# Optimization experiments

Measured on AMD Instinct MI355X. Metric: run time of the kernel, lower is better.

The kernel has to match this reference:

```python
import jax, jax.numpy as jnp
import numpy as np

EPS = 1e-08
N_HEADS = 8
WORD = 128
N_CELLS = 16384
BATCH = 16


def setup_inputs() -> dict:
    key = jax.random.key(0)
    k1, k2 = jax.random.split(key)
    memory = jax.random.normal(k1, (BATCH, N_CELLS, WORD), dtype=jnp.float32)
    controls = jax.random.normal(k2, (BATCH, N_HEADS * (WORD + 6)), dtype=jnp.float32)
    read_dist_bias = jnp.zeros((1, N_HEADS, N_CELLS), dtype=jnp.float32)
    return {"memory": memory, "controls": controls, "read_dist_bias": read_dist_bias}


def _split_controls(controls):
    # order: keys [B,H,W], betas [B,H,1], gates [B,H,1], shifts [B,H,3], gammas [B,H,1]
    B = controls.shape[0]
    pos = 0
    parts = []
    for size in (WORD, 1, 1, 3, 1):
        n = N_HEADS * size
        parts.append(controls[:, pos:pos + n].reshape(B, N_HEADS, size))
        pos += n
    return parts


def _circular_convolution(weights, shifts):
    # out[i] = w[(i-1)%C]*s0 + w[i]*s1 + w[(i+1)%C]*s2  (torch conv2d = cross-correlation)
    return (shifts[..., 0:1] * jnp.roll(weights, 1, axis=-1)
            + shifts[..., 1:2] * weights
            + shifts[..., 2:3] * jnp.roll(weights, -1, axis=-1))


def reference(memory, controls, read_dist_bias):
    keys, betas, gates, shifts, gammas = _split_controls(controls)
    keys = jnp.tanh(keys)                      # [B,H,W]
    betas = jax.nn.softplus(betas)             # [B,H,1]
    gates = jax.nn.sigmoid(gates)              # [B,H,1]
    shifts = jax.nn.softmax(shifts, axis=-1)   # [B,H,3]
    gammas = 1.0 + jax.nn.softplus(gammas)     # [B,H,1]

    # prev weights on a fresh sequence: softmax of the learned bias
    prev_weights = jax.nn.softmax(
        jnp.broadcast_to(read_dist_bias, (memory.shape[0], N_HEADS, N_CELLS)), axis=-1)

    # cosine similarity, [B,H,C]
    dots = jnp.einsum('bcw,bhw->bhc', memory, keys)
    norm = jnp.linalg.norm(keys, axis=-1)[..., None] * jnp.linalg.norm(memory, axis=-1)[:, None, :]
    scores = dots / (norm + EPS)

    w_content = jax.nn.softmax(scores * betas, axis=-1)
    w_interp = gates * w_content + (1.0 - gates) * prev_weights
    w_shift = _circular_convolution(w_interp, shifts)
    w_sharp = w_shift ** gammas
    read_dist = w_sharp / (jnp.sum(w_sharp, axis=-1, keepdims=True) + EPS)

    # read: [B,H,W]
    read_data = jnp.einsum('bhc,bcw->bhw', read_dist, memory)
    return read_data
```

## Files before the change

### kernel.cpp

```cpp
#include <hip/hip_runtime.h>

#define BATCH 16
#define HEADS 8
#define WORD  128
#define CELLS 16384
#define CTRL  1072
#define CB    256

__device__ __forceinline__ float softplusf(float x) {
  return (x > 20.f) ? x : log1pf(expf(x));
}

template<int OP>
__device__ __forceinline__ float block_reduce(float v, float* scratch) {
  #pragma unroll
  for (int o = 32; o > 0; o >>= 1) {
    float u = __shfl_xor(v, o, 64);
    v = OP ? fmaxf(v, u) : (v + u);
  }
  const int t = threadIdx.x;
  __syncthreads();
  if ((t & 63) == 0) scratch[t >> 6] = v;
  __syncthreads();
  if (t < 64) {
    v = (t < 16) ? scratch[t] : (OP ? -3.4e38f : 0.f);
    #pragma unroll
    for (int o = 8; o > 0; o >>= 1) {
      float u = __shfl_xor(v, o, 64);
      v = OP ? fmaxf(v, u) : (v + u);
    }
    if (t == 0) scratch[0] = v;
  }
  __syncthreads();
  v = scratch[0];
  __syncthreads();
  return v;
}

__global__ __launch_bounds__(256)
void scores_kernel(const float* __restrict__ mem,
                   const float* __restrict__ ctrl,
                   float* __restrict__ scores) {
  const int b = blockIdx.y;
  const int c = blockIdx.x * 256 + threadIdx.x;
  const int t = threadIdx.x;

  __shared__ float kk[HEADS * WORD];
  __shared__ float kn[HEADS];

  for (int i = t; i < HEADS * WORD; i += 256)
    kk[i] = tanhf(ctrl[b * CTRL + i]);
  __syncthreads();
  if (t < HEADS) {
    float s = 0.f;
    for (int w = 0; w < WORD; ++w) { float v = kk[t * WORD + w]; s += v * v; }
    kn[t] = sqrtf(s);
  }
  __syncthreads();

  float dot[HEADS];
  #pragma unroll
  for (int h = 0; h < HEADS; ++h) dot[h] = 0.f;
  float nm = 0.f;

  const float4* mrow = (const float4*)&mem[((size_t)b * CELLS + c) * WORD];
  const float4* k4   = (const float4*)kk;
  for (int w4 = 0; w4 < WORD / 4; ++w4) {
    float4 m = mrow[w4];
    nm = fmaf(m.x, m.x, fmaf(m.y, m.y, fmaf(m.z, m.z, fmaf(m.w, m.w, nm))));
    #pragma unroll
    for (int h = 0; h < HEADS; ++h) {
      float4 k = k4[h * (WORD / 4) + w4];
      dot[h] = fmaf(m.x, k.x, fmaf(m.y, k.y, fmaf(m.z, k.z, fmaf(m.w, k.w, dot[h]))));
    }
  }
  nm = sqrtf(nm);
  #pragma unroll
  for (int h = 0; h < HEADS; ++h)
    scores[((size_t)(b * HEADS + h)) * CELLS + c] = dot[h] / (kn[h] * nm + 1e-8f);
}

__global__ __launch_bounds__(1024)
void weights_kernel(const float* __restrict__ scores,
                    const float* __restrict__ ctrl,
                    const float* __restrict__ bias,
                    float* __restrict__ rd) {
  const int bh = blockIdx.x;
  const int b = bh >> 3, h = bh & 7;
  const int t = threadIdx.x;

  __shared__ float buf[CELLS];

  const float* cb = ctrl + b * CTRL;
  const float beta  = softplusf(cb[1024 + h]);
  const float gate  = 1.f / (1.f + expf(-cb[1032 + h]));
  float s0 = cb[1040 + h * 3 + 0];
  float s1 = cb[1040 + h * 3 + 1];
  float s2 = cb[1040 + h * 3 + 2];
  {
    float sm = fmaxf(s0, fmaxf(s1, s2));
    float e0 = expf(s0 - sm), e1 = expf(s1 - sm), e2 = expf(s2 - sm);
    float inv = 1.f / (e0 + e1 + e2);
    s0 = e0 * inv; s1 = e1 * inv; s2 = e2 * inv;
  }
  const float gamma = 1.f + softplusf(cb[1064 + h]);

  float x[16];
  const float* srow = scores + (size_t)bh * CELLS;
  #pragma unroll
  for (int i = 0; i < 16; ++i) x[i] = srow[t + i * 1024] * beta;
  float mx = x[0];
  #pragma unroll
  for (int i = 1; i < 16; ++i) mx = fmaxf(mx, x[i]);
  mx = block_reduce<1>(mx, buf);
  float se = 0.f;
  #pragma unroll
  for (int i = 0; i < 16; ++i) { x[i] = expf(x[i] - mx); se += x[i]; }
  se = block_reduce<0>(se, buf);

  float y[16];
  const float* brow = bias + (size_t)h * CELLS;
  #pragma unroll
  for (int i = 0; i < 16; ++i) y[i] = brow[t + i * 1024];
  float mb = y[0];
  #pragma unroll
  for (int i = 1; i < 16; ++i) mb = fmaxf(mb, y[i]);
  mb = block_reduce<1>(mb, buf);
  float sb = 0.f;
  #pragma unroll
  for (int i = 0; i < 16; ++i) { y[i] = expf(y[i] - mb); sb += y[i]; }
  sb = block_reduce<0>(sb, buf);

  const float a1 = gate / se;
  const float a2 = (1.f - gate) / sb;
  #pragma unroll
  for (int i = 0; i < 16; ++i)
    buf[t + i * 1024] = a1 * x[i] + a2 * y[i];
  __syncthreads();

  float sh[16]; float ss = 0.f;
  #pragma unroll
  for (int i = 0; i < 16; ++i) {
    int c = t + i * 1024;
    float wm = buf[(c + CELLS - 1) & (CELLS - 1)];
    float w0 = buf[c];
    float wp = buf[(c + 1) & (CELLS - 1)];
    float ws = fmaf(s0, wm, fmaf(s1, w0, s2 * wp));
    float p = powf(ws, gamma);
    sh[i] = p; ss += p;
  }
  ss = block_reduce<0>(ss, buf);
  const float inv = 1.f / (ss + 1e-8f);
  float* rrow = rd + (size_t)bh * CELLS;
  #pragma unroll
  for (int i = 0; i < 16; ++i) rrow[t + i * 1024] = sh[i] * inv;
}

__global__ __launch_bounds__(256)
void read_kernel(const float* __restrict__ mem,
                 const float* __restrict__ rd,
                 float* __restrict__ out) {
  const int b  = blockIdx.y;
  const int c0 = blockIdx.x * CB;
  const int t  = threadIdx.x;

  __shared__ float rds[HEADS][CB];
  __shared__ float red[8][HEADS * WORD];

  for (int i = t; i < HEADS * CB; i += 256)
    rds[i >> 8][i & 255] = rd[((size_t)b * HEADS + (i >> 8)) * CELLS + c0 + (i & 255)];
  __syncthreads();

  const int w4 = (t & 31) * 4;
  const int cc = t >> 5;
  float4 acc[HEADS];
  #pragma unroll
  for (int h = 0; h < HEADS; ++h) acc[h] = make_float4(0.f, 0.f, 0.f, 0.f);

  for (int c = cc; c < CB; c += 8) {
    float4 m = *(const float4*)&mem[((size_t)b * CELLS + c0 + c) * WORD + w4];
    #pragma unroll
    for (int h = 0; h < HEADS; ++h) {
      float r = rds[h][c];
      acc[h].x = fmaf(r, m.x, acc[h].x);
      acc[h].y = fmaf(r, m.y, acc[h].y);
      acc[h].z = fmaf(r, m.z, acc[h].z);
      acc[h].w = fmaf(r, m.w, acc[h].w);
    }
  }

  #pragma unroll
  for (int h = 0; h < HEADS; ++h)
    *(float4*)&red[cc][h * WORD + w4] = acc[h];
  __syncthreads();

  float4 s = *(float4*)&red[0][t * 4];
  #pragma unroll
  for (int c2 = 1; c2 < 8; ++c2) {
    float4 v = *(float4*)&red[c2][t * 4];
    s.x += v.x; s.y += v.y; s.z += v.z; s.w += v.w;
  }
  const int h = t >> 5;
  const int w = (t * 4) & 127;
  float* o = &out[((size_t)b * HEADS + h) * WORD + w];
  atomicAdd(o + 0, s.x);
  atomicAdd(o + 1, s.y);
  atomicAdd(o + 2, s.z);
  atomicAdd(o + 3, s.w);
}

extern "C" void kernel_launch(void* const* d_in, const int* in_sizes, int n_in,
                              void* d_out, int out_size, void* d_ws, size_t ws_size,
                              hipStream_t stream) {
  const float* mem  = (const float*)d_in[0];
  const float* ctrl = (const float*)d_in[1];
  const float* bias = (const float*)d_in[2];
  float* out    = (float*)d_out;
  float* scores = (float*)d_ws;
  float* rd     = scores + (size_t)BATCH * HEADS * CELLS;

  hipMemsetAsync(d_out, 0, sizeof(float) * BATCH * HEADS * WORD, stream);

  scores_kernel<<<dim3(CELLS / 256, BATCH), 256, 0, stream>>>(mem, ctrl, scores);
  weights_kernel<<<dim3(BATCH * HEADS), 1024, 0, stream>>>(scores, ctrl, bias, rd);
  read_kernel<<<dim3(CELLS / CB, BATCH), 256, 0, stream>>>(mem, rd, out);
}
```

Measured before the change: 271.0 us.

## Stage memory tiles in LDS for scores, precompute bias softmax, contiguous weight layout

```diff
diff --git a/kernel.cpp b/kernel.cpp
--- a/kernel.cpp
+++ b/kernel.cpp
@@ -5,10 +5,15 @@
 #define WORD  128
 #define CELLS 16384
 #define CTRL  1072
+#define K1_TILE 128
 #define CB    256
 
 __device__ __forceinline__ float softplusf(float x) {
   return (x > 20.f) ? x : log1pf(expf(x));
+}
+
+__device__ __forceinline__ float powpos(float ws, float g) {
+  return __builtin_amdgcn_exp2f(g * __builtin_amdgcn_logf(ws));
 }
 
 template<int OP>
@@ -23,7 +28,7 @@
   if ((t & 63) == 0) scratch[t >> 6] = v;
   __syncthreads();
   if (t < 64) {
-    v = (t < 16) ? scratch[t] : (OP ? -3.4e38f : 0.f);
+    v = (t < (int)(blockDim.x >> 6)) ? scratch[t] : (OP ? -3.4e38f : 0.f);
     #pragma unroll
     for (int o = 8; o > 0; o >>= 1) {
       float u = __shfl_xor(v, o, 64);
@@ -35,6 +40,37 @@
   v = scratch[0];
   __syncthreads();
   return v;
+}
+
+__global__ __launch_bounds__(1024)
+void bias_softmax_kernel(const float* __restrict__ bias, float* __restrict__ pw) {
+  __shared__ float red[16];
+  const int h = blockIdx.x, t = threadIdx.x;
+  const float4* b4 = (const float4*)(bias + (size_t)h * CELLS);
+  float4* p4 = (float4*)(pw + (size_t)h * CELLS);
+
+  float y[16];
+  #pragma unroll
+  for (int i4 = 0; i4 < 4; ++i4) {
+    float4 v = b4[t * 4 + i4];
+    y[i4*4+0] = v.x; y[i4*4+1] = v.y; y[i4*4+2] = v.z; y[i4*4+3] = v.w;
+  }
+  float m = y[0];
+  #pragma unroll
+  for (int i = 1; i < 16; ++i) m = fmaxf(m, y[i]);
+  m = block_reduce<1>(m, red);
+  float s = 0.f;
+  #pragma unroll
+  for (int i = 0; i < 16; ++i) {
+    y[i] = __builtin_amdgcn_exp2f((y[i] - m) * 1.442695040888963f);
+    s += y[i];
+  }
+  s = block_reduce<0>(s, red);
+  const float inv = 1.f / s;
+  #pragma unroll
+  for (int i4 = 0; i4 < 4; ++i4)
+    p4[t * 4 + i4] = make_float4(y[i4*4+0]*inv, y[i4*4+1]*inv,
+                                 y[i4*4+2]*inv, y[i4*4+3]*inv);
 }
 
 __global__ __launch_bounds__(256)
@@ -42,11 +78,11 @@
                    const float* __restrict__ ctrl,
                    float* __restrict__ scores) {
   const int b = blockIdx.y;
-  const int c = blockIdx.x * 256 + threadIdx.x;
   const int t = threadIdx.x;
 
-  __shared__ float kk[HEADS * WORD];
+  __shared__ __align__(16) float kk[HEADS * WORD];
   __shared__ float kn[HEADS];
+  __shared__ __align__(16) float tile[K1_TILE * WORD];
 
   for (int i = t; i < HEADS * WORD; i += 256)
     kk[i] = tanhf(ctrl[b * CTRL + i]);
@@ -56,40 +92,70 @@
     for (int w = 0; w < WORD; ++w) { float v = kk[t * WORD + w]; s += v * v; }
     kn[t] = sqrtf(s);
   }
-  __syncthreads();
-
-  float dot[HEADS];
-  #pragma unroll
-  for (int h = 0; h < HEADS; ++h) dot[h] = 0.f;
-  float nm = 0.f;
-
-  const float4* mrow = (const float4*)&mem[((size_t)b * CELLS + c) * WORD];
-  const float4* k4   = (const float4*)kk;
-  for (int w4 = 0; w4 < WORD / 4; ++w4) {
-    float4 m = mrow[w4];
-    nm = fmaf(m.x, m.x, fmaf(m.y, m.y, fmaf(m.z, m.z, fmaf(m.w, m.w, nm))));
-    #pragma unroll
-    for (int h = 0; h < HEADS; ++h) {
-      float4 k = k4[h * (WORD / 4) + w4];
-      dot[h] = fmaf(m.x, k.x, fmaf(m.y, k.y, fmaf(m.z, k.z, fmaf(m.w, k.w, dot[h]))));
-    }
-  }
-  nm = sqrtf(nm);
-  #pragma unroll
-  for (int h = 0; h < HEADS; ++h)
-    scores[((size_t)(b * HEADS + h)) * CELLS + c] = dot[h] / (kn[h] * nm + 1e-8f);
+
+  float4* tile4 = (float4*)tile;
+  const float4* gt4 =
+      (const float4*)(mem + ((size_t)b * CELLS + (size_t)blockIdx.x * K1_TILE) * WORD);
+  float4 stg[16];
+  #pragma unroll
+  for (int j = 0; j < 16; ++j) stg[j] = gt4[j * 256 + t];
+  #pragma unroll
+  for (int j = 0; j < 16; ++j) {
+    int i = j * 256 + t;
+    int r = i >> 5, c = i & 31;
+    tile4[r * 32 + (c ^ (r & 7))] = stg[j];
+  }
+  __syncthreads();
+
+  const float4* kk4 = (const float4*)kk;
+  const int quad = t >> 2, q = t & 3;
+  const size_t srow0 = (size_t)b * HEADS * CELLS + (size_t)blockIdx.x * K1_TILE;
+
+  #pragma unroll
+  for (int p = 0; p < 2; ++p) {
+    const int cell = p * 64 + quad;
+    float d[HEADS];
+    #pragma unroll
+    for (int h = 0; h < HEADS; ++h) d[h] = 0.f;
+    float nm = 0.f;
+
+    #pragma unroll
+    for (int jj = 0; jj < 8; ++jj) {
+      const int j = jj * 4 + q;
+      float4 m = tile4[cell * 32 + (j ^ (cell & 7))];
+      nm = fmaf(m.x, m.x, fmaf(m.y, m.y, fmaf(m.z, m.z, fmaf(m.w, m.w, nm))));
+      #pragma unroll
+      for (int h = 0; h < HEADS; ++h) {
+        float4 k = kk4[h * 32 + j];
+        d[h] = fmaf(m.x, k.x, fmaf(m.y, k.y, fmaf(m.z, k.z, fmaf(m.w, k.w, d[h]))));
+      }
+    }
+    #pragma unroll
+    for (int off = 1; off <= 2; off <<= 1) {
+      #pragma unroll
+      for (int h = 0; h < HEADS; ++h) d[h] += __shfl_xor(d[h], off);
+      nm += __shfl_xor(nm, off);
+    }
+    const float nmr = sqrtf(nm);
+    #pragma unroll
+    for (int u = 0; u < 2; ++u) {
+      const int h = q * 2 + u;
+      scores[srow0 + (size_t)h * CELLS + cell] = d[h] / (kn[h] * nmr + 1e-8f);
+    }
+  }
 }
 
 __global__ __launch_bounds__(1024)
 void weights_kernel(const float* __restrict__ scores,
                     const float* __restrict__ ctrl,
-                    const float* __restrict__ bias,
+                    const float* __restrict__ pw,
                     float* __restrict__ rd) {
   const int bh = blockIdx.x;
   const int b = bh >> 3, h = bh & 7;
   const int t = threadIdx.x;
 
-  __shared__ float buf[CELLS];
+  __shared__ float red[16];
+  __shared__ float wl[1024], wr[1024];
 
   const float* cb = ctrl + b * CTRL;
   const float beta  = softplusf(cb[1024 + h]);
@@ -105,55 +171,59 @@
   }
   const float gamma = 1.f + softplusf(cb[1064 + h]);
 
+  const float4* s4 = (const float4*)(scores + (size_t)bh * CELLS);
   float x[16];
-  const float* srow = scores + (size_t)bh * CELLS;
-  #pragma unroll
-  for (int i = 0; i < 16; ++i) x[i] = srow[t + i * 1024] * beta;
+  #pragma unroll
+  for (int i4 = 0; i4 < 4; ++i4) {
+    float4 v = s4[t * 4 + i4];
+    x[i4*4+0] = v.x * beta; x[i4*4+1] = v.y * beta;
+    x[i4*4+2] = v.z * beta; x[i4*4+3] = v.w * beta;
+  }
   float mx = x[0];
   #pragma unroll
   for (int i = 1; i < 16; ++i) mx = fmaxf(mx, x[i]);
-  mx = block_reduce<1>(mx, buf);
+  mx = block_reduce<1>(mx, red);
   float se = 0.f;
   #pragma unroll
-  for (int i = 0; i < 16; ++i) { x[i] = expf(x[i] - mx); se += x[i]; }
-  se = block_reduce<0>(se, buf);
-
-  float y[16];
-  const float* brow = bias + (size_t)h * CELLS;
-  #pragma unroll
-  for (int i = 0; i < 16; ++i) y[i] = brow[t + i * 1024];
-  float mb = y[0];
-  #pragma unroll
-  for (int i = 1; i < 16; ++i) mb = fmaxf(mb, y[i]);
-  mb = block_reduce<1>(mb, buf);
-  float sb = 0.f;
-  #pragma unroll
-  for (int i = 0; i < 16; ++i) { y[i] = expf(y[i] - mb); sb += y[i]; }
-  sb = block_reduce<0>(sb, buf);
-
+  for (int i = 0; i < 16; ++i) {
+    x[i] = __builtin_amdgcn_exp2f((x[i] - mx) * 1.442695040888963f);
+    se += x[i];
+  }
+  se = block_reduce<0>(se, red);
+
+  const float4* p4 = (const float4*)(pw + (size_t)h * CELLS);
   const float a1 = gate / se;
-  const float a2 = (1.f - gate) / sb;
-  #pragma unroll
-  for (int i = 0; i < 16; ++i)
-    buf[t + i * 1024] = a1 * x[i] + a2 * y[i];
-  __syncthreads();
-
+  const float a2 = 1.f - gate;
+  float wi[16];
+  #pragma unroll
+  for (int i4 = 0; i4 < 4; ++i4) {
+    float4 v = p4[t * 4 + i4];
+    wi[i4*4+0] = fmaf(a1, x[i4*4+0], a2 * v.x);
+    wi[i4*4+1] = fmaf(a1, x[i4*4+1], a2 * v.y);
+    wi[i4*4+2] = fmaf(a1, x[i4*4+2], a2 * v.z);
+    wi[i4*4+3] = fmaf(a1, x[i4*4+3], a2 * v.w);
+  }
+  wl[t] = wi[0]; wr[t] = wi[15];
+  __syncthreads();
+
+  const float wmE = wr[(t + 1023) & 1023];
+  const float wpE = wl[(t + 1)    & 1023];
   float sh[16]; float ss = 0.f;
   #pragma unroll
   for (int i = 0; i < 16; ++i) {
-    int c = t + i * 1024;
-    float wm = buf[(c + CELLS - 1) & (CELLS - 1)];
-    float w0 = buf[c];
-    float wp = buf[(c + 1) & (CELLS - 1)];
-    float ws = fmaf(s0, wm, fmaf(s1, w0, s2 * wp));
-    float p = powf(ws, gamma);
+    float wm = (i == 0)  ? wmE : wi[i - 1];
+    float wp = (i == 15) ? wpE : wi[i + 1];
+    float ws = fmaf(s0, wm, fmaf(s1, wi[i], s2 * wp));
+    float p = powpos(ws, gamma);
     sh[i] = p; ss += p;
   }
-  ss = block_reduce<0>(ss, buf);
+  ss = block_reduce<0>(ss, red);
   const float inv = 1.f / (ss + 1e-8f);
-  float* rrow = rd + (size_t)bh * CELLS;
-  #pragma unroll
-  for (int i = 0; i < 16; ++i) rrow[t + i * 1024] = sh[i] * inv;
+  float4* r4 = (float4*)(rd + (size_t)bh * CELLS);
+  #pragma unroll
+  for (int i4 = 0; i4 < 4; ++i4)
+    r4[t * 4 + i4] = make_float4(sh[i4*4+0]*inv, sh[i4*4+1]*inv,
+                                 sh[i4*4+2]*inv, sh[i4*4+3]*inv);
 }
 
 __global__ __launch_bounds__(256)
@@ -218,10 +288,12 @@
   float* out    = (float*)d_out;
   float* scores = (float*)d_ws;
   float* rd     = scores + (size_t)BATCH * HEADS * CELLS;
-
-  hipMemsetAsync(d_out, 0, sizeof(float) * BATCH * HEADS * WORD, stream);
-
-  scores_kernel<<<dim3(CELLS / 256, BATCH), 256, 0, stream>>>(mem, ctrl, scores);
-  weights_kernel<<<dim3(BATCH * HEADS), 1024, 0, stream>>>(scores, ctrl, bias, rd);
+  float* pw     = rd + (size_t)BATCH * HEADS * CELLS;
+
+  (void)hipMemsetAsync(d_out, 0, sizeof(float) * BATCH * HEADS * WORD, stream);
+
+  bias_softmax_kernel<<<dim3(HEADS), 1024, 0, stream>>>(bias, pw);
+  scores_kernel<<<dim3(CELLS / K1_TILE, BATCH), 256, 0, stream>>>(mem, ctrl, scores);
+  weights_kernel<<<dim3(BATCH * HEADS), 1024, 0, stream>>>(scores, ctrl, pw, rd);
   read_kernel<<<dim3(CELLS / CB, BATCH), 256, 0, stream>>>(mem, rd, out);
 }
```

Result: slower. 277.8 us (+2.5%).
